# Performance work log

Hardware: AMD Instinct MI355X
Metric: run time of the kernel (lower is better)

## Reference

```python
import jax, jax.numpy as jnp
import numpy as np

B, L, H, NH, NB = 16, 200, 128, 2, 2
ITEMS, SPAN = 50000, 256
NEG = -2.0**32 + 1.0  # mask value used by the torch module


def _ln(x, g, b, eps=1e-8):
    m = jnp.mean(x, axis=-1, keepdims=True)
    v = jnp.mean((x - m) ** 2, axis=-1, keepdims=True)
    return (x - m) / jnp.sqrt(v + eps) * g + b


def setup_inputs() -> dict:
    key = jax.random.key(0)
    ks = jax.random.split(key, 20)
    p = lambda k, s: (jax.random.normal(k, s, jnp.float32) * 0.02)
    item_emb = p(ks[0], (ITEMS + 1, H)).at[0].set(0.0)  # padding_idx=0
    return {
        "user_ids": jax.random.randint(ks[1], (B,), 0, 10000),
        "log_seqs": jax.random.randint(ks[2], (B, L), 0, ITEMS),
        "time_matrices": jax.random.randint(ks[3], (B, L, L), 0, SPAN),
        "pos_seqs": jax.random.randint(ks[4], (B, L), 0, ITEMS),
        "neg_seqs": jax.random.randint(ks[5], (B, L), 0, ITEMS),
        "item_emb": item_emb,
        "pos_K_emb": p(ks[6], (L, H)),
        "pos_V_emb": p(ks[7], (L, H)),
        "time_K_emb": p(ks[8], (SPAN + 1, H)),
        "time_V_emb": p(ks[9], (SPAN + 1, H)),
        "Wq": p(ks[10], (NB, H, H)), "bq": jnp.zeros((NB, H)),
        "Wk": p(ks[11], (NB, H, H)), "bk": jnp.zeros((NB, H)),
        "Wv": p(ks[12], (NB, H, H)), "bv": jnp.zeros((NB, H)),
        "ln1_g": jnp.ones((NB, H)), "ln1_b": jnp.zeros((NB, H)),
        "W1": p(ks[13], (NB, H, H)), "b1": jnp.zeros((NB, H)),
        "W2": p(ks[14], (NB, H, H)), "b2": jnp.zeros((NB, H)),
        "ln2_g": jnp.ones((NB, H)), "ln2_b": jnp.zeros((NB, H)),
        "lnf_g": jnp.ones((H,)), "lnf_b": jnp.zeros((H,)),
    }


def reference(user_ids, log_seqs, time_matrices, pos_seqs, neg_seqs,
              item_emb, pos_K_emb, pos_V_emb, time_K_emb, time_V_emb,
              Wq, bq, Wk, bk, Wv, bv, ln1_g, ln1_b,
              W1, b1, W2, b2, ln2_g, ln2_b, lnf_g, lnf_b):
    d = H // NH
    pad = (log_seqs == 0)                    # (B,L) timeline mask
    keep = (~pad)[..., None].astype(jnp.float32)

    seqs = item_emb[log_seqs] * jnp.sqrt(jnp.float32(H))
    seqs = seqs * keep
    posK = pos_K_emb.reshape(L, NH, d)       # same for every batch element
    posV = pos_V_emb.reshape(L, NH, d)
    tmK = time_K_emb[time_matrices].reshape(B, L, L, NH, d)  # (B,L,L,h,d)
    tmV = time_V_emb[time_matrices].reshape(B, L, L, NH, d)
    causal = ~jnp.tril(jnp.ones((L, L), dtype=bool))          # True = masked
    mask = pad[:, None, :, None] | causal[None, None, :, :]   # (B,1,L,L) row-mask | causal

    for i in range(NB):
        Q = (seqs @ Wq[i].T + bq[i]).reshape(B, L, NH, d)
        K = (seqs @ Wk[i].T + bk[i]).reshape(B, L, NH, d)
        V = (seqs @ Wv[i].T + bv[i]).reshape(B, L, NH, d)
        aw = jnp.einsum('bqhd,bkhd->bhqk', Q, K)
        aw = aw + jnp.einsum('bqhd,khd->bhqk', Q, posK)
        aw = aw + jnp.einsum('bqkhd,bqhd->bhqk', tmK, Q)
        aw = aw / jnp.sqrt(jnp.float32(d))
        aw = jnp.where(mask, NEG, aw)
        A = jax.nn.softmax(aw, axis=-1)                        # (B,h,L,L)
        out = jnp.einsum('bhqk,bkhd->bqhd', A, V)
        out = out + jnp.einsum('bhqk,khd->bqhd', A, posV)
        out = out + jnp.einsum('bhqk,bqkhd->bqhd', A, tmV)
        out = out.reshape(B, L, H)
        seqs = _ln(seqs + out, ln1_g[i], ln1_b[i])
        ffn = jax.nn.relu(seqs @ W1[i].T + b1[i]) @ W2[i].T + b2[i]
        seqs = _ln(seqs + ffn, ln2_g[i], ln2_b[i])
        seqs = seqs * keep

    log_feats = _ln(seqs, lnf_g, lnf_b)
    pos_logits = jnp.sum(log_feats * item_emb[pos_seqs], axis=-1)  # (B,L)
    neg_logits = jnp.sum(log_feats * item_emb[neg_seqs], axis=-1)
    return jnp.stack([pos_logits, neg_logits])  # (2,B,L)
```

## Files before the change

kernel.cpp:

```cpp
#include <hip/hip_runtime.h>
#include <hip/hip_bf16.h>
#include <math.h>

#define BB 16
#define LL 200
#define HH 128
#define DD 64
#define NQT 25
#define NEGF -4294967295.0f
#define SQRTH 11.313708498984761f

__global__ __launch_bounds__(512) void k_qkv(float* __restrict__ seqs,
    const int* __restrict__ log_seqs, const float* __restrict__ item_emb, int do_embed,
    const float* __restrict__ Wq, const float* __restrict__ bq,
    const float* __restrict__ Wk, const float* __restrict__ bk,
    const float* __restrict__ Wv, const float* __restrict__ bv,
    const float* __restrict__ posK, const float* __restrict__ posV,
    float* __restrict__ Q, float* __restrict__ Kp, float* __restrict__ Vp) {
    __shared__ float s_lds[16][HH];
    int r0g = blockIdx.x * 16;
    int t = threadIdx.x;
    if (do_embed) {
        int r = t >> 5, d4 = t & 31;
        int id = log_seqs[r0g + r];
        float4 v = make_float4(0.f, 0.f, 0.f, 0.f);
        if (id != 0) {
            v = ((const float4*)(item_emb + id * HH))[d4];
            v.x *= SQRTH; v.y *= SQRTH; v.z *= SQRTH; v.w *= SQRTH;
        }
        *(float4*)&s_lds[r][d4 * 4] = v;
        ((float4*)(seqs + r0g * HH))[t] = v;
    } else {
        ((float4*)s_lds)[t] = ((const float4*)(seqs + r0g * HH))[t];
    }
    __syncthreads();
    int c = t & 127, rg = t >> 7;
    float aq[4] = {0.f, 0.f, 0.f, 0.f};
    float ak[4] = {0.f, 0.f, 0.f, 0.f};
    float av[4] = {0.f, 0.f, 0.f, 0.f};
    const float4* wq4 = (const float4*)(Wq + c * HH);
    const float4* wk4 = (const float4*)(Wk + c * HH);
    const float4* wv4 = (const float4*)(Wv + c * HH);
#pragma unroll 4
    for (int k4 = 0; k4 < HH / 4; ++k4) {
        float4 wq = wq4[k4], wk = wk4[k4], wv = wv4[k4];
#pragma unroll
        for (int r = 0; r < 4; ++r) {
            float4 s = *(const float4*)&s_lds[rg * 4 + r][k4 * 4];
            aq[r] += s.x * wq.x + s.y * wq.y + s.z * wq.z + s.w * wq.w;
            ak[r] += s.x * wk.x + s.y * wk.y + s.z * wk.z + s.w * wk.w;
            av[r] += s.x * wv.x + s.y * wv.y + s.z * wv.z + s.w * wv.w;
        }
    }
#pragma unroll
    for (int r = 0; r < 4; ++r) {
        int row = r0g + rg * 4 + r;
        int l = row % LL;
        Q[row * HH + c]  = aq[r] + bq[c];
        Kp[row * HH + c] = ak[r] + bk[c] + posK[l * HH + c];
        Vp[row * HH + c] = av[r] + bv[c] + posV[l * HH + c];
    }
}

__global__ __launch_bounds__(256) void k_proj(const float* __restrict__ Q,
    const float* __restrict__ timeK, float* __restrict__ projK) {
    int bh = blockIdx.x / 25, qt = blockIdx.x % 25;
    int b = bh >> 1, h = bh & 1;
    int qlo = qt * 8;
    __shared__ float Qs[8][68];
    __shared__ float TK[2][32][68];
    int t = threadIdx.x;
    if (t < 128) {
        int r = t >> 4, d4 = t & 15;
        *(float4*)&Qs[r][d4 * 4] =
            ((const float4*)(Q + (b * LL + qlo + r) * HH + h * DD))[d4];
    }
    for (int x = t; x < 512; x += 256) {
        int i = x >> 4, d4 = x & 15;
        *(float4*)&TK[0][i][d4 * 4] =
            ((const float4*)(timeK + i * HH + h * DD))[d4];
    }
    int tq = t >> 5, ttl = t & 31;
    for (int ch = 0; ch < 9; ++ch) {
        __syncthreads();
        if (ch + 1 < 9) {
            int nb = (ch + 1) * 32;
            for (int x = t; x < 512; x += 256) {
                int i = x >> 4, d4 = x & 15;
                int tt = nb + i;
                if (tt < 257)
                    *(float4*)&TK[(ch + 1) & 1][i][d4 * 4] =
                        ((const float4*)(timeK + tt * HH + h * DD))[d4];
            }
        }
        int tt = ch * 32 + ttl;
        if (tt < 257) {
            float acc = 0.f;
#pragma unroll
            for (int d4 = 0; d4 < 16; ++d4) {
                float4 qv = *(const float4*)&Qs[tq][d4 * 4];
                float4 kv = *(const float4*)&TK[ch & 1][ttl][d4 * 4];
                acc += qv.x * kv.x + qv.y * kv.y + qv.z * kv.z + qv.w * kv.w;
            }
            projK[(bh * LL + qlo + tq) * 257 + tt] = acc;
        }
    }
}

__global__ __launch_bounds__(256) void k_attn(
    const float* __restrict__ Q, const float* __restrict__ Kp, const float* __restrict__ Vp,
    const float* __restrict__ projK, const float* __restrict__ timeV,
    const int* __restrict__ tm, const int* __restrict__ log_seqs,
    float* __restrict__ attnout) {
    int bh = blockIdx.x / NQT, qt = blockIdx.x % NQT;
    int b = bh >> 1, h = bh & 1;
    int qlo = qt * 8;
    __shared__ float K_s[2][32][68];
    __shared__ float smemW[457 * 12];
    __shared__ int s_allmask;
#define WT(i, j) smemW[(i) * 12 + (j)]
    int t = threadIdx.x;
    int tq = t >> 5, lane = t & 31, g = tq;
    int q = qlo + tq;
    int qhi = qlo + 7;

    if (t == 0) s_allmask = 0;
    for (int x = 200 * 12 + t; x < 457 * 12; x += 256) smemW[x] = 0.f;
    float4 qreg[16];
    {
        const float4* qp = (const float4*)(Q + (b * LL + q) * HH + h * DD);
#pragma unroll
        for (int d4 = 0; d4 < 16; ++d4) qreg[d4] = qp[d4];
    }
    const int* tmrow = tm + (b * LL + q) * LL;
    const float* projrow = projK + (bh * LL + q) * 257;
    const int* lsrow = log_seqs + b * LL;

    for (int x = t; x < 512; x += 256) {
        int i = x >> 4, d4 = x & 15;
        *(float4*)&K_s[0][i][d4 * 4] =
            ((const float4*)(Kp + (b * LL + i) * HH + h * DD))[d4];
    }

    float s[7];
#pragma unroll
    for (int j = 0; j < 7; ++j) s[j] = NEGF;
    int nkc = (qhi >> 5) + 1;
#pragma unroll
    for (int kc = 0; kc < 7; ++kc) {
        if (kc < nkc) {
            __syncthreads();
            if (kc + 1 < nkc) {
                int kb = (kc + 1) * 32;
                for (int x = t; x < 512; x += 256) {
                    int i = x >> 4, d4 = x & 15;
                    int k = kb + i;
                    if (k < LL)
                        *(float4*)&K_s[(kc + 1) & 1][i][d4 * 4] =
                            ((const float4*)(Kp + (b * LL + k) * HH + h * DD))[d4];
                }
            }
            int k = kc * 32 + lane;
            if (k <= q && lsrow[k] != 0) {
                float acc = 0.f;
#pragma unroll
                for (int d4 = 0; d4 < 16; ++d4) {
                    float4 kv = *(const float4*)&K_s[kc & 1][lane][d4 * 4];
                    acc += qreg[d4].x * kv.x + qreg[d4].y * kv.y +
                           qreg[d4].z * kv.z + qreg[d4].w * kv.w;
                }
                s[kc] = (acc + projrow[tmrow[k]]) * 0.125f;
            }
        }
    }

    float mx = s[0];
#pragma unroll
    for (int j = 1; j < 7; ++j) mx = fmaxf(mx, s[j]);
    mx = fmaxf(mx, __shfl_xor(mx, 1, 64));
    mx = fmaxf(mx, __shfl_xor(mx, 2, 64));
    mx = fmaxf(mx, __shfl_xor(mx, 4, 64));
    mx = fmaxf(mx, __shfl_xor(mx, 8, 64));
    mx = fmaxf(mx, __shfl_xor(mx, 16, 64));
    bool allmask = (mx == NEGF);
    float sum = 0.f;
#pragma unroll
    for (int j = 0; j < 7; ++j) {
        int k = lane + 32 * j;
        float e = (k < LL) ? __expf(s[j] - mx) : 0.f;
        s[j] = e;
        sum += e;
    }
    sum += __shfl_xor(sum, 1, 64);
    sum += __shfl_xor(sum, 2, 64);
    sum += __shfl_xor(sum, 4, 64);
    sum += __shfl_xor(sum, 8, 64);
    sum += __shfl_xor(sum, 16, 64);
    float inv = 1.0f / sum;
    int klim = allmask ? LL : (q + 1);
    if (allmask && lane == 0) s_allmask = 1;
#pragma unroll
    for (int j = 0; j < 7; ++j) {
        int k = lane + 32 * j;
        if (k < LL) {
            float p = s[j] * inv;
            WT(k, tq) = p;
            if (k < klim && p != 0.f)
                atomicAdd(&WT(200 + tmrow[k], tq), p);
        }
    }
    __syncthreads();

    int kmax = s_allmask ? LL : (qhi + 1);
    float a00=0.f,a01=0.f,a10=0.f,a11=0.f,a20=0.f,a21=0.f,a30=0.f,a31=0.f;
    float a40=0.f,a41=0.f,a50=0.f,a51=0.f,a60=0.f,a61=0.f,a70=0.f,a71=0.f;
#define PV_STEP(WROW, SRCPTR)                                            \
    {                                                                    \
        const float* wr = &WROW;                                         \
        float4 w0 = *(const float4*)wr;                                  \
        float4 w1 = *(const float4*)(wr + 4);                            \
        float2 vv = *(const float2*)(SRCPTR);                            \
        a00 += w0.x * vv.x; a01 += w0.x * vv.y;                          \
        a10 += w0.y * vv.x; a11 += w0.y * vv.y;                          \
        a20 += w0.z * vv.x; a21 += w0.z * vv.y;                          \
        a30 += w0.w * vv.x; a31 += w0.w * vv.y;                          \
        a40 += w1.x * vv.x; a41 += w1.x * vv.y;                          \
        a50 += w1.y * vv.x; a51 += w1.y * vv.y;                          \
        a60 += w1.z * vv.x; a61 += w1.z * vv.y;                          \
        a70 += w1.w * vv.x; a71 += w1.w * vv.y;                          \
    }
    for (int i = g; i < kmax; i += 8)
        PV_STEP(WT(i, 0), Vp + (b * LL + i) * HH + h * DD + lane * 2);
    for (int i = g; i < 257; i += 8)
        PV_STEP(WT(200 + i, 0), timeV + i * HH + h * DD + lane * 2);
#undef PV_STEP
    __syncthreads();
    float* part = smemW;
    part[g * 512 + 0 * 64 + lane * 2] = a00; part[g * 512 + 0 * 64 + lane * 2 + 1] = a01;
    part[g * 512 + 1 * 64 + lane * 2] = a10; part[g * 512 + 1 * 64 + lane * 2 + 1] = a11;
    part[g * 512 + 2 * 64 + lane * 2] = a20; part[g * 512 + 2 * 64 + lane * 2 + 1] = a21;
    part[g * 512 + 3 * 64 + lane * 2] = a30; part[g * 512 + 3 * 64 + lane * 2 + 1] = a31;
    part[g * 512 + 4 * 64 + lane * 2] = a40; part[g * 512 + 4 * 64 + lane * 2 + 1] = a41;
    part[g * 512 + 5 * 64 + lane * 2] = a50; part[g * 512 + 5 * 64 + lane * 2 + 1] = a51;
    part[g * 512 + 6 * 64 + lane * 2] = a60; part[g * 512 + 6 * 64 + lane * 2 + 1] = a61;
    part[g * 512 + 7 * 64 + lane * 2] = a70; part[g * 512 + 7 * 64 + lane * 2 + 1] = a71;
    __syncthreads();
    {
        float ox = 0.f, oy = 0.f;
#pragma unroll
        for (int gg = 0; gg < 8; ++gg) {
            ox += part[gg * 512 + tq * 64 + lane * 2];
            oy += part[gg * 512 + tq * 64 + lane * 2 + 1];
        }
        *(float2*)(attnout + (b * LL + q) * HH + h * DD + lane * 2) =
            make_float2(ox, oy);
    }
#undef WT
}

__global__ __launch_bounds__(512) void k_ffn_full(
    float* __restrict__ seqs, const float* __restrict__ AO,
    const float* __restrict__ g1, const float* __restrict__ be1,
    const float* __restrict__ W1, const float* __restrict__ b1,
    const float* __restrict__ W2, const float* __restrict__ b2,
    const float* __restrict__ g2, const float* __restrict__ be2,
    const int* __restrict__ log_seqs, int do_final,
    const float* __restrict__ lnf_g, const float* __restrict__ lnf_b,
    const float* __restrict__ item_emb,
    const int* __restrict__ pos_seqs, const int* __restrict__ neg_seqs,
    float* __restrict__ out) {
    __shared__ float s_lds[16][HH];
    __shared__ float h_lds[16][HH];
    int r0g = blockIdx.x * 16;
    int t = threadIdx.x;
    {
        float4 a = ((const float4*)(seqs + r0g * HH))[t];
        float4 o = ((const float4*)(AO + r0g * HH))[t];
        a.x += o.x; a.y += o.y; a.z += o.z; a.w += o.w;
        ((float4*)s_lds)[t] = a;
    }
    __syncthreads();
    int w = t >> 6, lane = t & 63;
    int lrow = w * 2 + (lane >> 5), cl = lane & 31;
    {
        float sm = 0.f;
#pragma unroll
        for (int j = 0; j < 4; ++j) sm += s_lds[lrow][cl + 32 * j];
        sm += __shfl_xor(sm, 1, 64);  sm += __shfl_xor(sm, 2, 64);
        sm += __shfl_xor(sm, 4, 64);  sm += __shfl_xor(sm, 8, 64);
        sm += __shfl_xor(sm, 16, 64);
        float mean = sm * (1.0f / HH);
        float vr = 0.f;
#pragma unroll
        for (int j = 0; j < 4; ++j) {
            float d = s_lds[lrow][cl + 32 * j] - mean;
            vr += d * d;
        }
        vr += __shfl_xor(vr, 1, 64);  vr += __shfl_xor(vr, 2, 64);
        vr += __shfl_xor(vr, 4, 64);  vr += __shfl_xor(vr, 8, 64);
        vr += __shfl_xor(vr, 16, 64);
        float rstd = rsqrtf(vr * (1.0f / HH) + 1e-8f);
#pragma unroll
        for (int j = 0; j < 4; ++j) {
            int c = cl + 32 * j;
            s_lds[lrow][c] = (s_lds[lrow][c] - mean) * rstd * g1[c] + be1[c];
        }
    }
    __syncthreads();
    int c = t & 127, rg = t >> 7;
    float acc[4] = {0.f, 0.f, 0.f, 0.f};
    const float4* w14 = (const float4*)(W1 + c * HH);
#pragma unroll 4
    for (int k4 = 0; k4 < HH / 4; ++k4) {
        float4 ww = w14[k4];
#pragma unroll
        for (int r = 0; r < 4; ++r) {
            float4 s = *(const float4*)&s_lds[rg * 4 + r][k4 * 4];
            acc[r] += s.x * ww.x + s.y * ww.y + s.z * ww.z + s.w * ww.w;
        }
    }
#pragma unroll
    for (int r = 0; r < 4; ++r) h_lds[rg * 4 + r][c] = fmaxf(acc[r] + b1[c], 0.f);
    __syncthreads();
#pragma unroll
    for (int r = 0; r < 4; ++r) acc[r] = 0.f;
    const float4* w24 = (const float4*)(W2 + c * HH);
#pragma unroll 4
    for (int k4 = 0; k4 < HH / 4; ++k4) {
        float4 ww = w24[k4];
#pragma unroll
        for (int r = 0; r < 4; ++r) {
            float4 s = *(const float4*)&h_lds[rg * 4 + r][k4 * 4];
            acc[r] += s.x * ww.x + s.y * ww.y + s.z * ww.z + s.w * ww.w;
        }
    }
    __syncthreads();
#pragma unroll
    for (int r = 0; r < 4; ++r)
        h_lds[rg * 4 + r][c] = s_lds[rg * 4 + r][c] + acc[r] + b2[c];
    __syncthreads();
    {
        float sm = 0.f;
#pragma unroll
        for (int j = 0; j < 4; ++j) sm += h_lds[lrow][cl + 32 * j];
        sm += __shfl_xor(sm, 1, 64);  sm += __shfl_xor(sm, 2, 64);
        sm += __shfl_xor(sm, 4, 64);  sm += __shfl_xor(sm, 8, 64);
        sm += __shfl_xor(sm, 16, 64);
        float mean = sm * (1.0f / HH);
        float vr = 0.f;
#pragma unroll
        for (int j = 0; j < 4; ++j) {
            float d = h_lds[lrow][cl + 32 * j] - mean;
            vr += d * d;
        }
        vr += __shfl_xor(vr, 1, 64);  vr += __shfl_xor(vr, 2, 64);
        vr += __shfl_xor(vr, 4, 64);  vr += __shfl_xor(vr, 8, 64);
        vr += __shfl_xor(vr, 16, 64);
        float rstd = rsqrtf(vr * (1.0f / HH) + 1e-8f);
        int row = r0g + lrow;
        float keep = (log_seqs[row] != 0) ? 1.0f : 0.0f;
        float y2[4];
#pragma unroll
        for (int j = 0; j < 4; ++j) {
            int cc = cl + 32 * j;
            y2[j] = ((h_lds[lrow][cc] - mean) * rstd * g2[cc] + be2[cc]) * keep;
        }
        if (!do_final) {
#pragma unroll
            for (int j = 0; j < 4; ++j)
                seqs[row * HH + cl + 32 * j] = y2[j];
        } else {
            float sm2 = y2[0] + y2[1] + y2[2] + y2[3];
            sm2 += __shfl_xor(sm2, 1, 64);  sm2 += __shfl_xor(sm2, 2, 64);
            sm2 += __shfl_xor(sm2, 4, 64);  sm2 += __shfl_xor(sm2, 8, 64);
            sm2 += __shfl_xor(sm2, 16, 64);
            float mean2 = sm2 * (1.0f / HH);
            float vr2 = 0.f;
#pragma unroll
            for (int j = 0; j < 4; ++j) {
                float d = y2[j] - mean2;
                vr2 += d * d;
            }
            vr2 += __shfl_xor(vr2, 1, 64);  vr2 += __shfl_xor(vr2, 2, 64);
            vr2 += __shfl_xor(vr2, 4, 64);  vr2 += __shfl_xor(vr2, 8, 64);
            vr2 += __shfl_xor(vr2, 16, 64);
            float rstd2 = rsqrtf(vr2 * (1.0f / HH) + 1e-8f);
            int pid = pos_seqs[row];
            int nid = neg_seqs[row];
            float pp = 0.f, nn = 0.f;
#pragma unroll
            for (int j = 0; j < 4; ++j) {
                int cc = cl + 32 * j;
                float lf = (y2[j] - mean2) * rstd2 * lnf_g[cc] + lnf_b[cc];
                pp += lf * item_emb[pid * HH + cc];
                nn += lf * item_emb[nid * HH + cc];
            }
            pp += __shfl_xor(pp, 1, 64);  pp += __shfl_xor(pp, 2, 64);
            pp += __shfl_xor(pp, 4, 64);  pp += __shfl_xor(pp, 8, 64);
            pp += __shfl_xor(pp, 16, 64);
            nn += __shfl_xor(nn, 1, 64);  nn += __shfl_xor(nn, 2, 64);
            nn += __shfl_xor(nn, 4, 64);  nn += __shfl_xor(nn, 8, 64);
            nn += __shfl_xor(nn, 16, 64);
            if (cl == 0) {
                out[row] = pp;
                out[BB * LL + row] = nn;
            }
        }
    }
}

extern "C" void kernel_launch(void* const* d_in, const int* in_sizes, int n_in,
                              void* d_out, int out_size, void* d_ws, size_t ws_size,
                              hipStream_t stream) {
    const int* log_seqs = (const int*)d_in[1];
    const int* tm       = (const int*)d_in[2];
    const int* pos_seqs = (const int*)d_in[3];
    const int* neg_seqs = (const int*)d_in[4];
    const float* item_emb = (const float*)d_in[5];
    const float* posK   = (const float*)d_in[6];
    const float* posV   = (const float*)d_in[7];
    const float* timeK  = (const float*)d_in[8];
    const float* timeV  = (const float*)d_in[9];
    const float* Wq = (const float*)d_in[10];
    const float* bq = (const float*)d_in[11];
    const float* Wk = (const float*)d_in[12];
    const float* bk = (const float*)d_in[13];
    const float* Wv = (const float*)d_in[14];
    const float* bv = (const float*)d_in[15];
    const float* ln1_g = (const float*)d_in[16];
    const float* ln1_b = (const float*)d_in[17];
    const float* W1 = (const float*)d_in[18];
    const float* b1 = (const float*)d_in[19];
    const float* W2 = (const float*)d_in[20];
    const float* b2 = (const float*)d_in[21];
    const float* ln2_g = (const float*)d_in[22];
    const float* ln2_b = (const float*)d_in[23];
    const float* lnf_g = (const float*)d_in[24];
    const float* lnf_b = (const float*)d_in[25];

    float* ws    = (float*)d_ws;
    float* seqs  = ws;
    float* Qb    = seqs + 409600;
    float* Kpb   = Qb + 409600;
    float* Vpb   = Kpb + 409600;
    float* AO    = Vpb + 409600;
    float* projK = AO + 409600;

    for (int i = 0; i < 2; ++i) {
        k_qkv<<<BB * LL / 16, 512, 0, stream>>>(seqs, log_seqs, item_emb,
            (i == 0) ? 1 : 0,
            Wq + i * HH * HH, bq + i * HH,
            Wk + i * HH * HH, bk + i * HH,
            Wv + i * HH * HH, bv + i * HH,
            posK, posV, Qb, Kpb, Vpb);
        k_proj<<<32 * NQT, 256, 0, stream>>>(Qb, timeK, projK);
        k_attn<<<32 * NQT, 256, 0, stream>>>(Qb, Kpb, Vpb, projK, timeV,
                                             tm, log_seqs, AO);
        k_ffn_full<<<BB * LL / 16, 512, 0, stream>>>(seqs, AO,
            ln1_g + i * HH, ln1_b + i * HH,
            W1 + i * HH * HH, b1 + i * HH,
            W2 + i * HH * HH, b2 + i * HH,
            ln2_g + i * HH, ln2_b + i * HH, log_seqs,
            (i == 1) ? 1 : 0, lnf_g, lnf_b, item_emb,
            pos_seqs, neg_seqs, (float*)d_out);
    }
}
```

Before: 186.1 us.

## Fuse all layer stages into one cooperative persistent kernel with grid syncs

Replaces the eight separate kernel launches (qkv, proj, attn, ffn for each of two layers) with a single cooperative persistent kernel that loops over tiles and uses grid-wide barriers between phases. The goal is to remove per-launch overhead and the idle gaps between dependent kernels. In exchange, all phases now run with 256 threads and 8-row tiles instead of 512 threads and 16-row tiles. The attention K-tile loading also loses its double buffering and adds an extra barrier per chunk. Grid-sync cost and the reduced occupancy, set by the shared smem footprint, could offset the gains.

```diff
diff --git a/kernel.cpp b/kernel.cpp
--- a/kernel.cpp
+++ b/kernel.cpp
@@ -1,6 +1,8 @@
 #include <hip/hip_runtime.h>
-#include <hip/hip_bf16.h>
+#include <hip/hip_cooperative_groups.h>
 #include <math.h>
+
+namespace cg = cooperative_groups;
 
 #define BB 16
 #define LL 200
@@ -10,30 +12,42 @@
 #define NEGF -4294967295.0f
 #define SQRTH 11.313708498984761f
 
-__global__ __launch_bounds__(512) void k_qkv(float* __restrict__ seqs,
-    const int* __restrict__ log_seqs, const float* __restrict__ item_emb, int do_embed,
-    const float* __restrict__ Wq, const float* __restrict__ bq,
-    const float* __restrict__ Wk, const float* __restrict__ bk,
-    const float* __restrict__ Wv, const float* __restrict__ bv,
-    const float* __restrict__ posK, const float* __restrict__ posV,
-    float* __restrict__ Q, float* __restrict__ Kp, float* __restrict__ Vp) {
-    __shared__ float s_lds[16][HH];
-    int r0g = blockIdx.x * 16;
+struct Params {
+    const int* log_seqs; const int* tm; const int* pos_seqs; const int* neg_seqs;
+    const float* item_emb; const float* posK; const float* posV;
+    const float* timeK; const float* timeV;
+    const float* Wq; const float* bq; const float* Wk; const float* bk;
+    const float* Wv; const float* bv;
+    const float* ln1_g; const float* ln1_b;
+    const float* W1; const float* b1; const float* W2; const float* b2;
+    const float* ln2_g; const float* ln2_b;
+    const float* lnf_g; const float* lnf_b;
+    float* seqs; float* Q; float* Kp; float* Vp; float* AO; float* projK;
+    float* out;
+};
+
+__device__ void ph_qkv(const Params& P, float* smem, int tile, int layer) {
+    float (*s_lds)[HH] = (float (*)[HH])smem;
+    int r0g = tile * 8;
     int t = threadIdx.x;
-    if (do_embed) {
+    __syncthreads();
+    if (layer == 0) {
         int r = t >> 5, d4 = t & 31;
-        int id = log_seqs[r0g + r];
+        int id = P.log_seqs[r0g + r];
         float4 v = make_float4(0.f, 0.f, 0.f, 0.f);
         if (id != 0) {
-            v = ((const float4*)(item_emb + id * HH))[d4];
+            v = ((const float4*)(P.item_emb + id * HH))[d4];
             v.x *= SQRTH; v.y *= SQRTH; v.z *= SQRTH; v.w *= SQRTH;
         }
         *(float4*)&s_lds[r][d4 * 4] = v;
-        ((float4*)(seqs + r0g * HH))[t] = v;
+        ((float4*)(P.seqs + r0g * HH))[t] = v;
     } else {
-        ((float4*)s_lds)[t] = ((const float4*)(seqs + r0g * HH))[t];
-    }
-    __syncthreads();
+        ((float4*)s_lds)[t] = ((const float4*)(P.seqs + r0g * HH))[t];
+    }
+    __syncthreads();
+    const float* Wq = P.Wq + layer * HH * HH; const float* bq = P.bq + layer * HH;
+    const float* Wk = P.Wk + layer * HH * HH; const float* bk = P.bk + layer * HH;
+    const float* Wv = P.Wv + layer * HH * HH; const float* bv = P.bv + layer * HH;
     int c = t & 127, rg = t >> 7;
     float aq[4] = {0.f, 0.f, 0.f, 0.f};
     float ak[4] = {0.f, 0.f, 0.f, 0.f};
@@ -56,29 +70,29 @@
     for (int r = 0; r < 4; ++r) {
         int row = r0g + rg * 4 + r;
         int l = row % LL;
-        Q[row * HH + c]  = aq[r] + bq[c];
-        Kp[row * HH + c] = ak[r] + bk[c] + posK[l * HH + c];
-        Vp[row * HH + c] = av[r] + bv[c] + posV[l * HH + c];
-    }
-}
-
-__global__ __launch_bounds__(256) void k_proj(const float* __restrict__ Q,
-    const float* __restrict__ timeK, float* __restrict__ projK) {
-    int bh = blockIdx.x / 25, qt = blockIdx.x % 25;
+        P.Q[row * HH + c]  = aq[r] + bq[c];
+        P.Kp[row * HH + c] = ak[r] + bk[c] + P.posK[l * HH + c];
+        P.Vp[row * HH + c] = av[r] + bv[c] + P.posV[l * HH + c];
+    }
+}
+
+__device__ void ph_proj(const Params& P, float* smem, int tile) {
+    float (*Qs)[68] = (float (*)[68])smem;
+    float (*TK)[32][68] = (float (*)[32][68])(smem + 544);
+    int bh = tile / NQT, qt = tile % NQT;
     int b = bh >> 1, h = bh & 1;
     int qlo = qt * 8;
-    __shared__ float Qs[8][68];
-    __shared__ float TK[2][32][68];
     int t = threadIdx.x;
+    __syncthreads();
     if (t < 128) {
         int r = t >> 4, d4 = t & 15;
         *(float4*)&Qs[r][d4 * 4] =
-            ((const float4*)(Q + (b * LL + qlo + r) * HH + h * DD))[d4];
+            ((const float4*)(P.Q + (b * LL + qlo + r) * HH + h * DD))[d4];
     }
     for (int x = t; x < 512; x += 256) {
         int i = x >> 4, d4 = x & 15;
         *(float4*)&TK[0][i][d4 * 4] =
-            ((const float4*)(timeK + i * HH + h * DD))[d4];
+            ((const float4*)(P.timeK + i * HH + h * DD))[d4];
     }
     int tq = t >> 5, ttl = t & 31;
     for (int ch = 0; ch < 9; ++ch) {
@@ -90,7 +104,7 @@
                 int tt = nb + i;
                 if (tt < 257)
                     *(float4*)&TK[(ch + 1) & 1][i][d4 * 4] =
-                        ((const float4*)(timeK + tt * HH + h * DD))[d4];
+                        ((const float4*)(P.timeK + tt * HH + h * DD))[d4];
             }
         }
         int tt = ch * 32 + ttl;
@@ -102,45 +116,34 @@
                 float4 kv = *(const float4*)&TK[ch & 1][ttl][d4 * 4];
                 acc += qv.x * kv.x + qv.y * kv.y + qv.z * kv.z + qv.w * kv.w;
             }
-            projK[(bh * LL + qlo + tq) * 257 + tt] = acc;
-        }
-    }
-}
-
-__global__ __launch_bounds__(256) void k_attn(
-    const float* __restrict__ Q, const float* __restrict__ Kp, const float* __restrict__ Vp,
-    const float* __restrict__ projK, const float* __restrict__ timeV,
-    const int* __restrict__ tm, const int* __restrict__ log_seqs,
-    float* __restrict__ attnout) {
-    int bh = blockIdx.x / NQT, qt = blockIdx.x % NQT;
+            P.projK[(bh * LL + qlo + tq) * 257 + tt] = acc;
+        }
+    }
+}
+
+__device__ void ph_attn(const Params& P, float* smem, int* s_allmask_p, int tile) {
+    float (*K_s)[68] = (float (*)[68])smem;
+    float* smemW = smem + 2176;
+#define WT(i, j) smemW[(i) * 12 + (j)]
+    int bh = tile / NQT, qt = tile % NQT;
     int b = bh >> 1, h = bh & 1;
     int qlo = qt * 8;
-    __shared__ float K_s[2][32][68];
-    __shared__ float smemW[457 * 12];
-    __shared__ int s_allmask;
-#define WT(i, j) smemW[(i) * 12 + (j)]
     int t = threadIdx.x;
     int tq = t >> 5, lane = t & 31, g = tq;
     int q = qlo + tq;
     int qhi = qlo + 7;
-
-    if (t == 0) s_allmask = 0;
+    __syncthreads();
+    if (t == 0) *s_allmask_p = 0;
     for (int x = 200 * 12 + t; x < 457 * 12; x += 256) smemW[x] = 0.f;
     float4 qreg[16];
     {
-        const float4* qp = (const float4*)(Q + (b * LL + q) * HH + h * DD);
+        const float4* qp = (const float4*)(P.Q + (b * LL + q) * HH + h * DD);
 #pragma unroll
         for (int d4 = 0; d4 < 16; ++d4) qreg[d4] = qp[d4];
     }
-    const int* tmrow = tm + (b * LL + q) * LL;
-    const float* projrow = projK + (bh * LL + q) * 257;
-    const int* lsrow = log_seqs + b * LL;
-
-    for (int x = t; x < 512; x += 256) {
-        int i = x >> 4, d4 = x & 15;
-        *(float4*)&K_s[0][i][d4 * 4] =
-            ((const float4*)(Kp + (b * LL + i) * HH + h * DD))[d4];
-    }
+    const int* tmrow = P.tm + (b * LL + q) * LL;
+    const float* projrow = P.projK + (bh * LL + q) * 257;
+    const int* lsrow = P.log_seqs + b * LL;
 
     float s[7];
 #pragma unroll
@@ -149,28 +152,27 @@
 #pragma unroll
     for (int kc = 0; kc < 7; ++kc) {
         if (kc < nkc) {
+            int kbase = kc * 32;
+            for (int x = t; x < 512; x += 256) {
+                int i = x >> 4, d4 = x & 15;
+                int k = kbase + i;
+                if (k < LL)
+                    *(float4*)&K_s[i][d4 * 4] =
+                        ((const float4*)(P.Kp + (b * LL + k) * HH + h * DD))[d4];
+            }
             __syncthreads();
-            if (kc + 1 < nkc) {
-                int kb = (kc + 1) * 32;
-                for (int x = t; x < 512; x += 256) {
-                    int i = x >> 4, d4 = x & 15;
-                    int k = kb + i;
-                    if (k < LL)
-                        *(float4*)&K_s[(kc + 1) & 1][i][d4 * 4] =
-                            ((const float4*)(Kp + (b * LL + k) * HH + h * DD))[d4];
-                }
-            }
-            int k = kc * 32 + lane;
+            int k = kbase + lane;
             if (k <= q && lsrow[k] != 0) {
                 float acc = 0.f;
 #pragma unroll
                 for (int d4 = 0; d4 < 16; ++d4) {
-                    float4 kv = *(const float4*)&K_s[kc & 1][lane][d4 * 4];
+                    float4 kv = *(const float4*)&K_s[lane][d4 * 4];
                     acc += qreg[d4].x * kv.x + qreg[d4].y * kv.y +
                            qreg[d4].z * kv.z + qreg[d4].w * kv.w;
                 }
                 s[kc] = (acc + projrow[tmrow[k]]) * 0.125f;
             }
+            __syncthreads();
         }
     }
 
@@ -198,7 +200,7 @@
     sum += __shfl_xor(sum, 16, 64);
     float inv = 1.0f / sum;
     int klim = allmask ? LL : (q + 1);
-    if (allmask && lane == 0) s_allmask = 1;
+    if (allmask && lane == 0) *s_allmask_p = 1;
 #pragma unroll
     for (int j = 0; j < 7; ++j) {
         int k = lane + 32 * j;
@@ -211,7 +213,7 @@
     }
     __syncthreads();
 
-    int kmax = s_allmask ? LL : (qhi + 1);
+    int kmax = (*s_allmask_p) ? LL : (qhi + 1);
     float a00=0.f,a01=0.f,a10=0.f,a11=0.f,a20=0.f,a21=0.f,a30=0.f,a31=0.f;
     float a40=0.f,a41=0.f,a50=0.f,a51=0.f,a60=0.f,a61=0.f,a70=0.f,a71=0.f;
 #define PV_STEP(WROW, SRCPTR)                                            \
@@ -230,9 +232,9 @@
         a70 += w1.w * vv.x; a71 += w1.w * vv.y;                          \
     }
     for (int i = g; i < kmax; i += 8)
-        PV_STEP(WT(i, 0), Vp + (b * LL + i) * HH + h * DD + lane * 2);
+        PV_STEP(WT(i, 0), P.Vp + (b * LL + i) * HH + h * DD + lane * 2);
     for (int i = g; i < 257; i += 8)
-        PV_STEP(WT(200 + i, 0), timeV + i * HH + h * DD + lane * 2);
+        PV_STEP(WT(200 + i, 0), P.timeV + i * HH + h * DD + lane * 2);
 #undef PV_STEP
     __syncthreads();
     float* part = smemW;
@@ -252,30 +254,26 @@
             ox += part[gg * 512 + tq * 64 + lane * 2];
             oy += part[gg * 512 + tq * 64 + lane * 2 + 1];
         }
-        *(float2*)(attnout + (b * LL + q) * HH + h * DD + lane * 2) =
+        *(float2*)(P.AO + (b * LL + q) * HH + h * DD + lane * 2) =
             make_float2(ox, oy);
     }
 #undef WT
 }
 
-__global__ __launch_bounds__(512) void k_ffn_full(
-    float* __restrict__ seqs, const float* __restrict__ AO,
-    const float* __restrict__ g1, const float* __restrict__ be1,
-    const float* __restrict__ W1, const float* __restrict__ b1,
-    const float* __restrict__ W2, const float* __restrict__ b2,
-    const float* __restrict__ g2, const float* __restrict__ be2,
-    const int* __restrict__ log_seqs, int do_final,
-    const float* __restrict__ lnf_g, const float* __restrict__ lnf_b,
-    const float* __restrict__ item_emb,
-    const int* __restrict__ pos_seqs, const int* __restrict__ neg_seqs,
-    float* __restrict__ out) {
-    __shared__ float s_lds[16][HH];
-    __shared__ float h_lds[16][HH];
-    int r0g = blockIdx.x * 16;
+__device__ void ph_ffn(const Params& P, float* smem, int tile, int layer) {
+    float (*s_lds)[HH] = (float (*)[HH])smem;
+    float (*h_lds)[HH] = (float (*)[HH])(smem + 1024);
+    int r0g = tile * 8;
     int t = threadIdx.x;
+    int do_final = (layer == 1);
+    const float* g1  = P.ln1_g + layer * HH; const float* be1 = P.ln1_b + layer * HH;
+    const float* W1  = P.W1 + layer * HH * HH; const float* b1 = P.b1 + layer * HH;
+    const float* W2  = P.W2 + layer * HH * HH; const float* b2 = P.b2 + layer * HH;
+    const float* g2  = P.ln2_g + layer * HH; const float* be2 = P.ln2_b + layer * HH;
+    __syncthreads();
     {
-        float4 a = ((const float4*)(seqs + r0g * HH))[t];
-        float4 o = ((const float4*)(AO + r0g * HH))[t];
+        float4 a = ((const float4*)(P.seqs + r0g * HH))[t];
+        float4 o = ((const float4*)(P.AO + r0g * HH))[t];
         a.x += o.x; a.y += o.y; a.z += o.z; a.w += o.w;
         ((float4*)s_lds)[t] = a;
     }
@@ -358,7 +356,7 @@
         vr += __shfl_xor(vr, 16, 64);
         float rstd = rsqrtf(vr * (1.0f / HH) + 1e-8f);
         int row = r0g + lrow;
-        float keep = (log_seqs[row] != 0) ? 1.0f : 0.0f;
+        float keep = (P.log_seqs[row] != 0) ? 1.0f : 0.0f;
         float y2[4];
 #pragma unroll
         for (int j = 0; j < 4; ++j) {
@@ -368,7 +366,7 @@
         if (!do_final) {
 #pragma unroll
             for (int j = 0; j < 4; ++j)
-                seqs[row * HH + cl + 32 * j] = y2[j];
+                P.seqs[row * HH + cl + 32 * j] = y2[j];
         } else {
             float sm2 = y2[0] + y2[1] + y2[2] + y2[3];
             sm2 += __shfl_xor(sm2, 1, 64);  sm2 += __shfl_xor(sm2, 2, 64);
@@ -385,15 +383,15 @@
             vr2 += __shfl_xor(vr2, 4, 64);  vr2 += __shfl_xor(vr2, 8, 64);
             vr2 += __shfl_xor(vr2, 16, 64);
             float rstd2 = rsqrtf(vr2 * (1.0f / HH) + 1e-8f);
-            int pid = pos_seqs[row];
-            int nid = neg_seqs[row];
+            int pid = P.pos_seqs[row];
+            int nid = P.neg_seqs[row];
             float pp = 0.f, nn = 0.f;
 #pragma unroll
             for (int j = 0; j < 4; ++j) {
                 int cc = cl + 32 * j;
-                float lf = (y2[j] - mean2) * rstd2 * lnf_g[cc] + lnf_b[cc];
-                pp += lf * item_emb[pid * HH + cc];
-                nn += lf * item_emb[nid * HH + cc];
+                float lf = (y2[j] - mean2) * rstd2 * P.lnf_g[cc] + P.lnf_b[cc];
+                pp += lf * P.item_emb[pid * HH + cc];
+                nn += lf * P.item_emb[nid * HH + cc];
             }
             pp += __shfl_xor(pp, 1, 64);  pp += __shfl_xor(pp, 2, 64);
             pp += __shfl_xor(pp, 4, 64);  pp += __shfl_xor(pp, 8, 64);
@@ -402,66 +400,72 @@
             nn += __shfl_xor(nn, 4, 64);  nn += __shfl_xor(nn, 8, 64);
             nn += __shfl_xor(nn, 16, 64);
             if (cl == 0) {
-                out[row] = pp;
-                out[BB * LL + row] = nn;
-            }
-        }
+                P.out[row] = pp;
+                P.out[BB * LL + row] = nn;
+            }
+        }
+    }
+}
+
+__global__ __launch_bounds__(256, 4) void k_mega(Params P) {
+    cg::grid_group grid = cg::this_grid();
+    __shared__ float smem[7660];
+    __shared__ int s_allmask;
+    for (int layer = 0; layer < 2; ++layer) {
+        for (int tile = blockIdx.x; tile < 400; tile += gridDim.x)
+            ph_qkv(P, smem, tile, layer);
+        grid.sync();
+        for (int tile = blockIdx.x; tile < 800; tile += gridDim.x)
+            ph_proj(P, smem, tile);
+        grid.sync();
+        for (int tile = blockIdx.x; tile < 800; tile += gridDim.x)
+            ph_attn(P, smem, &s_allmask, tile);
+        grid.sync();
+        for (int tile = blockIdx.x; tile < 400; tile += gridDim.x)
+            ph_ffn(P, smem, tile, layer);
+        if (layer == 0) grid.sync();
     }
 }
 
 extern "C" void kernel_launch(void* const* d_in, const int* in_sizes, int n_in,
                               void* d_out, int out_size, void* d_ws, size_t ws_size,
                               hipStream_t stream) {
-    const int* log_seqs = (const int*)d_in[1];
-    const int* tm       = (const int*)d_in[2];
-    const int* pos_seqs = (const int*)d_in[3];
-    const int* neg_seqs = (const int*)d_in[4];
-    const float* item_emb = (const float*)d_in[5];
-    const float* posK   = (const float*)d_in[6];
-    const float* posV   = (const float*)d_in[7];
-    const float* timeK  = (const float*)d_in[8];
-    const float* timeV  = (const float*)d_in[9];
-    const float* Wq = (const float*)d_in[10];
-    const float* bq = (const float*)d_in[11];
-    const float* Wk = (const float*)d_in[12];
-    const float* bk = (const float*)d_in[13];
-    const float* Wv = (const float*)d_in[14];
-    const float* bv = (const float*)d_in[15];
-    const float* ln1_g = (const float*)d_in[16];
-    const float* ln1_b = (const float*)d_in[17];
-    const float* W1 = (const float*)d_in[18];
-    const float* b1 = (const float*)d_in[19];
-    const float* W2 = (const float*)d_in[20];
-    const float* b2 = (const float*)d_in[21];
-    const float* ln2_g = (const float*)d_in[22];
-    const float* ln2_b = (const float*)d_in[23];
-    const float* lnf_g = (const float*)d_in[24];
-    const float* lnf_b = (const float*)d_in[25];
-
-    float* ws    = (float*)d_ws;
-    float* seqs  = ws;
-    float* Qb    = seqs + 409600;
-    float* Kpb   = Qb + 409600;
-    float* Vpb   = Kpb + 409600;
-    float* AO    = Vpb + 409600;
-    float* projK = AO + 409600;
-
-    for (int i = 0; i < 2; ++i) {
-        k_qkv<<<BB * LL / 16, 512, 0, stream>>>(seqs, log_seqs, item_emb,
-            (i == 0) ? 1 : 0,
-            Wq + i * HH * HH, bq + i * HH,
-            Wk + i * HH * HH, bk + i * HH,
-            Wv + i * HH * HH, bv + i * HH,
-            posK, posV, Qb, Kpb, Vpb);
-        k_proj<<<32 * NQT, 256, 0, stream>>>(Qb, timeK, projK);
-        k_attn<<<32 * NQT, 256, 0, stream>>>(Qb, Kpb, Vpb, projK, timeV,
-                                             tm, log_seqs, AO);
-        k_ffn_full<<<BB * LL / 16, 512, 0, stream>>>(seqs, AO,
-            ln1_g + i * HH, ln1_b + i * HH,
-            W1 + i * HH * HH, b1 + i * HH,
-            W2 + i * HH * HH, b2 + i * HH,
-            ln2_g + i * HH, ln2_b + i * HH, log_seqs,
-            (i == 1) ? 1 : 0, lnf_g, lnf_b, item_emb,
-            pos_seqs, neg_seqs, (float*)d_out);
-    }
-}
+    Params P;
+    P.log_seqs = (const int*)d_in[1];
+    P.tm       = (const int*)d_in[2];
+    P.pos_seqs = (const int*)d_in[3];
+    P.neg_seqs = (const int*)d_in[4];
+    P.item_emb = (const float*)d_in[5];
+    P.posK  = (const float*)d_in[6];
+    P.posV  = (const float*)d_in[7];
+    P.timeK = (const float*)d_in[8];
+    P.timeV = (const float*)d_in[9];
+    P.Wq = (const float*)d_in[10]; P.bq = (const float*)d_in[11];
+    P.Wk = (const float*)d_in[12]; P.bk = (const float*)d_in[13];
+    P.Wv = (const float*)d_in[14]; P.bv = (const float*)d_in[15];
+    P.ln1_g = (const float*)d_in[16]; P.ln1_b = (const float*)d_in[17];
+    P.W1 = (const float*)d_in[18]; P.b1 = (const float*)d_in[19];
+    P.W2 = (const float*)d_in[20]; P.b2 = (const float*)d_in[21];
+    P.ln2_g = (const float*)d_in[22]; P.ln2_b = (const float*)d_in[23];
+    P.lnf_g = (const float*)d_in[24]; P.lnf_b = (const float*)d_in[25];
+
+    float* ws = (float*)d_ws;
+    P.seqs  = ws;
+    P.Q     = ws + 409600;
+    P.Kp    = ws + 2 * 409600;
+    P.Vp    = ws + 3 * 409600;
+    P.AO    = ws + 4 * 409600;
+    P.projK = ws + 5 * 409600;
+    P.out   = (float*)d_out;
+
+    int maxBlk = 0;
+    if (hipOccupancyMaxActiveBlocksPerMultiprocessor(&maxBlk, (const void*)k_mega,
+                                                     256, 0) != hipSuccess || maxBlk < 1)
+        maxBlk = 1;
+    unsigned grid = (unsigned)maxBlk * 256u;
+    if (grid > 800u) grid = 800u;
+
+    void* args[] = { (void*)&P };
+    hipLaunchCooperativeKernel((const void*)k_mega, dim3(grid), dim3(256),
+                               args, 0, stream);
+}
```

Measured after the change: 660.4 us. 3.55x slower.

## Drop double buffering in proj/attn and retile FFN to four rows per block

Applied to the files above, without the earlier changes.

The time-embedding and key tile loads in k_proj and k_attn go from double-buffered prefetch to single-buffered load-then-sync loops, which halves their shared memory but removes load/compute overlap and adds a barrier per chunk. The FFN kernel now handles 4 rows per 512-thread block instead of 16, so it launches 800 blocks instead of 200. Each thread computes one output column for one row, and layernorm reductions span the full 64-lane wavefront. More blocks spread the work across more CUs, but W1/W2 reuse per block drops fourfold.

```diff
diff --git a/kernel.cpp b/kernel.cpp
--- a/kernel.cpp
+++ b/kernel.cpp
@@ -68,38 +68,32 @@
     int b = bh >> 1, h = bh & 1;
     int qlo = qt * 8;
     __shared__ float Qs[8][68];
-    __shared__ float TK[2][32][68];
+    __shared__ float TK[32][68];
     int t = threadIdx.x;
     if (t < 128) {
         int r = t >> 4, d4 = t & 15;
         *(float4*)&Qs[r][d4 * 4] =
             ((const float4*)(Q + (b * LL + qlo + r) * HH + h * DD))[d4];
     }
-    for (int x = t; x < 512; x += 256) {
-        int i = x >> 4, d4 = x & 15;
-        *(float4*)&TK[0][i][d4 * 4] =
-            ((const float4*)(timeK + i * HH + h * DD))[d4];
-    }
     int tq = t >> 5, ttl = t & 31;
     for (int ch = 0; ch < 9; ++ch) {
+        int base = ch * 32;
         __syncthreads();
-        if (ch + 1 < 9) {
-            int nb = (ch + 1) * 32;
-            for (int x = t; x < 512; x += 256) {
-                int i = x >> 4, d4 = x & 15;
-                int tt = nb + i;
-                if (tt < 257)
-                    *(float4*)&TK[(ch + 1) & 1][i][d4 * 4] =
-                        ((const float4*)(timeK + tt * HH + h * DD))[d4];
-            }
-        }
-        int tt = ch * 32 + ttl;
+        for (int x = t; x < 512; x += 256) {
+            int i = x >> 4, d4 = x & 15;
+            int tt = base + i;
+            if (tt < 257)
+                *(float4*)&TK[i][d4 * 4] =
+                    ((const float4*)(timeK + tt * HH + h * DD))[d4];
+        }
+        __syncthreads();
+        int tt = base + ttl;
         if (tt < 257) {
             float acc = 0.f;
 #pragma unroll
             for (int d4 = 0; d4 < 16; ++d4) {
                 float4 qv = *(const float4*)&Qs[tq][d4 * 4];
-                float4 kv = *(const float4*)&TK[ch & 1][ttl][d4 * 4];
+                float4 kv = *(const float4*)&TK[ttl][d4 * 4];
                 acc += qv.x * kv.x + qv.y * kv.y + qv.z * kv.z + qv.w * kv.w;
             }
             projK[(bh * LL + qlo + tq) * 257 + tt] = acc;
@@ -115,7 +109,7 @@
     int bh = blockIdx.x / NQT, qt = blockIdx.x % NQT;
     int b = bh >> 1, h = bh & 1;
     int qlo = qt * 8;
-    __shared__ float K_s[2][32][68];
+    __shared__ float K_s[32][68];
     __shared__ float smemW[457 * 12];
     __shared__ int s_allmask;
 #define WT(i, j) smemW[(i) * 12 + (j)]
@@ -136,12 +130,6 @@
     const float* projrow = projK + (bh * LL + q) * 257;
     const int* lsrow = log_seqs + b * LL;
 
-    for (int x = t; x < 512; x += 256) {
-        int i = x >> 4, d4 = x & 15;
-        *(float4*)&K_s[0][i][d4 * 4] =
-            ((const float4*)(Kp + (b * LL + i) * HH + h * DD))[d4];
-    }
-
     float s[7];
 #pragma unroll
     for (int j = 0; j < 7; ++j) s[j] = NEGF;
@@ -149,28 +137,27 @@
 #pragma unroll
     for (int kc = 0; kc < 7; ++kc) {
         if (kc < nkc) {
+            int kbase = kc * 32;
+            for (int x = t; x < 512; x += 256) {
+                int i = x >> 4, d4 = x & 15;
+                int k = kbase + i;
+                if (k < LL)
+                    *(float4*)&K_s[i][d4 * 4] =
+                        ((const float4*)(Kp + (b * LL + k) * HH + h * DD))[d4];
+            }
             __syncthreads();
-            if (kc + 1 < nkc) {
-                int kb = (kc + 1) * 32;
-                for (int x = t; x < 512; x += 256) {
-                    int i = x >> 4, d4 = x & 15;
-                    int k = kb + i;
-                    if (k < LL)
-                        *(float4*)&K_s[(kc + 1) & 1][i][d4 * 4] =
-                            ((const float4*)(Kp + (b * LL + k) * HH + h * DD))[d4];
-                }
-            }
-            int k = kc * 32 + lane;
+            int k = kbase + lane;
             if (k <= q && lsrow[k] != 0) {
                 float acc = 0.f;
 #pragma unroll
                 for (int d4 = 0; d4 < 16; ++d4) {
-                    float4 kv = *(const float4*)&K_s[kc & 1][lane][d4 * 4];
+                    float4 kv = *(const float4*)&K_s[lane][d4 * 4];
                     acc += qreg[d4].x * kv.x + qreg[d4].y * kv.y +
                            qreg[d4].z * kv.z + qreg[d4].w * kv.w;
                 }
                 s[kc] = (acc + projrow[tmrow[k]]) * 0.125f;
             }
+            __syncthreads();
         }
     }
 
@@ -258,7 +245,7 @@
 #undef WT
 }
 
-__global__ __launch_bounds__(512) void k_ffn_full(
+__global__ __launch_bounds__(512) void k_ffn(
     float* __restrict__ seqs, const float* __restrict__ AO,
     const float* __restrict__ g1, const float* __restrict__ be1,
     const float* __restrict__ W1, const float* __restrict__ b1,
@@ -269,141 +256,116 @@
     const float* __restrict__ item_emb,
     const int* __restrict__ pos_seqs, const int* __restrict__ neg_seqs,
     float* __restrict__ out) {
-    __shared__ float s_lds[16][HH];
-    __shared__ float h_lds[16][HH];
-    int r0g = blockIdx.x * 16;
+    __shared__ float s_lds[4][HH];
+    __shared__ float h_lds[4][HH];
+    int r0g = blockIdx.x * 4;
     int t = threadIdx.x;
-    {
+    int wv = t >> 6, lane = t & 63;
+    int lrow = wv >> 1, par = wv & 1;
+
+    if (t < 128) {
         float4 a = ((const float4*)(seqs + r0g * HH))[t];
         float4 o = ((const float4*)(AO + r0g * HH))[t];
         a.x += o.x; a.y += o.y; a.z += o.z; a.w += o.w;
         ((float4*)s_lds)[t] = a;
     }
     __syncthreads();
-    int w = t >> 6, lane = t & 63;
-    int lrow = w * 2 + (lane >> 5), cl = lane & 31;
-    {
-        float sm = 0.f;
-#pragma unroll
-        for (int j = 0; j < 4; ++j) sm += s_lds[lrow][cl + 32 * j];
+    {
+        float x0 = s_lds[lrow][lane], x1 = s_lds[lrow][lane + 64];
+        float sm = x0 + x1;
         sm += __shfl_xor(sm, 1, 64);  sm += __shfl_xor(sm, 2, 64);
         sm += __shfl_xor(sm, 4, 64);  sm += __shfl_xor(sm, 8, 64);
-        sm += __shfl_xor(sm, 16, 64);
+        sm += __shfl_xor(sm, 16, 64); sm += __shfl_xor(sm, 32, 64);
         float mean = sm * (1.0f / HH);
-        float vr = 0.f;
-#pragma unroll
-        for (int j = 0; j < 4; ++j) {
-            float d = s_lds[lrow][cl + 32 * j] - mean;
-            vr += d * d;
-        }
+        float d0 = x0 - mean, d1 = x1 - mean;
+        float vr = d0 * d0 + d1 * d1;
         vr += __shfl_xor(vr, 1, 64);  vr += __shfl_xor(vr, 2, 64);
         vr += __shfl_xor(vr, 4, 64);  vr += __shfl_xor(vr, 8, 64);
-        vr += __shfl_xor(vr, 16, 64);
+        vr += __shfl_xor(vr, 16, 64); vr += __shfl_xor(vr, 32, 64);
         float rstd = rsqrtf(vr * (1.0f / HH) + 1e-8f);
-#pragma unroll
-        for (int j = 0; j < 4; ++j) {
-            int c = cl + 32 * j;
-            s_lds[lrow][c] = (s_lds[lrow][c] - mean) * rstd * g1[c] + be1[c];
-        }
-    }
-    __syncthreads();
-    int c = t & 127, rg = t >> 7;
-    float acc[4] = {0.f, 0.f, 0.f, 0.f};
-    const float4* w14 = (const float4*)(W1 + c * HH);
-#pragma unroll 4
-    for (int k4 = 0; k4 < HH / 4; ++k4) {
-        float4 ww = w14[k4];
-#pragma unroll
-        for (int r = 0; r < 4; ++r) {
-            float4 s = *(const float4*)&s_lds[rg * 4 + r][k4 * 4];
-            acc[r] += s.x * ww.x + s.y * ww.y + s.z * ww.z + s.w * ww.w;
-        }
-    }
-#pragma unroll
-    for (int r = 0; r < 4; ++r) h_lds[rg * 4 + r][c] = fmaxf(acc[r] + b1[c], 0.f);
-    __syncthreads();
-#pragma unroll
-    for (int r = 0; r < 4; ++r) acc[r] = 0.f;
-    const float4* w24 = (const float4*)(W2 + c * HH);
-#pragma unroll 4
-    for (int k4 = 0; k4 < HH / 4; ++k4) {
-        float4 ww = w24[k4];
-#pragma unroll
-        for (int r = 0; r < 4; ++r) {
-            float4 s = *(const float4*)&h_lds[rg * 4 + r][k4 * 4];
-            acc[r] += s.x * ww.x + s.y * ww.y + s.z * ww.z + s.w * ww.w;
-        }
-    }
-    __syncthreads();
-#pragma unroll
-    for (int r = 0; r < 4; ++r)
-        h_lds[rg * 4 + r][c] = s_lds[rg * 4 + r][c] + acc[r] + b2[c];
-    __syncthreads();
-    {
-        float sm = 0.f;
-#pragma unroll
-        for (int j = 0; j < 4; ++j) sm += h_lds[lrow][cl + 32 * j];
+        int cw = lane + par * 64;
+        float dn = par ? d1 : d0;
+        __syncthreads();
+        s_lds[lrow][cw] = dn * rstd * g1[cw] + be1[cw];
+    }
+    __syncthreads();
+    int row = t >> 7, col = t & 127;
+    {
+        float acc = 0.f;
+        const float4* w4 = (const float4*)(W1 + col * HH);
+        const float4* s4 = (const float4*)&s_lds[row][0];
+#pragma unroll 8
+        for (int k4 = 0; k4 < 32; ++k4) {
+            float4 w = w4[k4];
+            float4 s = s4[k4];
+            acc += s.x * w.x + s.y * w.y + s.z * w.z + s.w * w.w;
+        }
+        h_lds[row][col] = fmaxf(acc + b1[col], 0.f);
+    }
+    __syncthreads();
+    float x2;
+    {
+        float acc = 0.f;
+        const float4* w4 = (const float4*)(W2 + col * HH);
+        const float4* h4 = (const float4*)&h_lds[row][0];
+#pragma unroll 8
+        for (int k4 = 0; k4 < 32; ++k4) {
+            float4 w = w4[k4];
+            float4 s = h4[k4];
+            acc += s.x * w.x + s.y * w.y + s.z * w.z + s.w * w.w;
+        }
+        x2 = s_lds[row][col] + acc + b2[col];
+    }
+    __syncthreads();
+    h_lds[row][col] = x2;
+    __syncthreads();
+    {
+        float x0 = h_lds[lrow][lane], x1 = h_lds[lrow][lane + 64];
+        float sm = x0 + x1;
         sm += __shfl_xor(sm, 1, 64);  sm += __shfl_xor(sm, 2, 64);
         sm += __shfl_xor(sm, 4, 64);  sm += __shfl_xor(sm, 8, 64);
-        sm += __shfl_xor(sm, 16, 64);
+        sm += __shfl_xor(sm, 16, 64); sm += __shfl_xor(sm, 32, 64);
         float mean = sm * (1.0f / HH);
-        float vr = 0.f;
-#pragma unroll
-        for (int j = 0; j < 4; ++j) {
-            float d = h_lds[lrow][cl + 32 * j] - mean;
-            vr += d * d;
-        }
+        float d0 = x0 - mean, d1 = x1 - mean;
+        float vr = d0 * d0 + d1 * d1;
         vr += __shfl_xor(vr, 1, 64);  vr += __shfl_xor(vr, 2, 64);
         vr += __shfl_xor(vr, 4, 64);  vr += __shfl_xor(vr, 8, 64);
-        vr += __shfl_xor(vr, 16, 64);
+        vr += __shfl_xor(vr, 16, 64); vr += __shfl_xor(vr, 32, 64);
         float rstd = rsqrtf(vr * (1.0f / HH) + 1e-8f);
-        int row = r0g + lrow;
-        float keep = (log_seqs[row] != 0) ? 1.0f : 0.0f;
-        float y2[4];
-#pragma unroll
-        for (int j = 0; j < 4; ++j) {
-            int cc = cl + 32 * j;
-            y2[j] = ((h_lds[lrow][cc] - mean) * rstd * g2[cc] + be2[cc]) * keep;
-        }
+        int grow = r0g + lrow;
+        float keep = (log_seqs[grow] != 0) ? 1.0f : 0.0f;
+        float y0 = (d0 * rstd * g2[lane] + be2[lane]) * keep;
+        float y1 = (d1 * rstd * g2[lane + 64] + be2[lane + 64]) * keep;
         if (!do_final) {
-#pragma unroll
-            for (int j = 0; j < 4; ++j)
-                seqs[row * HH + cl + 32 * j] = y2[j];
+            if (par == 0) seqs[grow * HH + lane] = y0;
+            else          seqs[grow * HH + lane + 64] = y1;
         } else {
-            float sm2 = y2[0] + y2[1] + y2[2] + y2[3];
+            float sm2 = y0 + y1;
             sm2 += __shfl_xor(sm2, 1, 64);  sm2 += __shfl_xor(sm2, 2, 64);
             sm2 += __shfl_xor(sm2, 4, 64);  sm2 += __shfl_xor(sm2, 8, 64);
-            sm2 += __shfl_xor(sm2, 16, 64);
+            sm2 += __shfl_xor(sm2, 16, 64); sm2 += __shfl_xor(sm2, 32, 64);
             float mean2 = sm2 * (1.0f / HH);
-            float vr2 = 0.f;
-#pragma unroll
-            for (int j = 0; j < 4; ++j) {
-                float d = y2[j] - mean2;
-                vr2 += d * d;
-            }
+            float e0 = y0 - mean2, e1 = y1 - mean2;
+            float vr2 = e0 * e0 + e1 * e1;
             vr2 += __shfl_xor(vr2, 1, 64);  vr2 += __shfl_xor(vr2, 2, 64);
             vr2 += __shfl_xor(vr2, 4, 64);  vr2 += __shfl_xor(vr2, 8, 64);
-            vr2 += __shfl_xor(vr2, 16, 64);
+            vr2 += __shfl_xor(vr2, 16, 64); vr2 += __shfl_xor(vr2, 32, 64);
             float rstd2 = rsqrtf(vr2 * (1.0f / HH) + 1e-8f);
-            int pid = pos_seqs[row];
-            int nid = neg_seqs[row];
-            float pp = 0.f, nn = 0.f;
-#pragma unroll
-            for (int j = 0; j < 4; ++j) {
-                int cc = cl + 32 * j;
-                float lf = (y2[j] - mean2) * rstd2 * lnf_g[cc] + lnf_b[cc];
-                pp += lf * item_emb[pid * HH + cc];
-                nn += lf * item_emb[nid * HH + cc];
-            }
+            int pid = pos_seqs[grow];
+            int nid = neg_seqs[grow];
+            float lf0 = e0 * rstd2 * lnf_g[lane] + lnf_b[lane];
+            float lf1 = e1 * rstd2 * lnf_g[lane + 64] + lnf_b[lane + 64];
+            float pp = lf0 * item_emb[pid * HH + lane] + lf1 * item_emb[pid * HH + lane + 64];
+            float nn = lf0 * item_emb[nid * HH + lane] + lf1 * item_emb[nid * HH + lane + 64];
             pp += __shfl_xor(pp, 1, 64);  pp += __shfl_xor(pp, 2, 64);
             pp += __shfl_xor(pp, 4, 64);  pp += __shfl_xor(pp, 8, 64);
-            pp += __shfl_xor(pp, 16, 64);
+            pp += __shfl_xor(pp, 16, 64); pp += __shfl_xor(pp, 32, 64);
             nn += __shfl_xor(nn, 1, 64);  nn += __shfl_xor(nn, 2, 64);
             nn += __shfl_xor(nn, 4, 64);  nn += __shfl_xor(nn, 8, 64);
-            nn += __shfl_xor(nn, 16, 64);
-            if (cl == 0) {
-                out[row] = pp;
-                out[BB * LL + row] = nn;
+            nn += __shfl_xor(nn, 16, 64); nn += __shfl_xor(nn, 32, 64);
+            if (par == 0 && lane == 0) {
+                out[grow] = pp;
+                out[BB * LL + grow] = nn;
             }
         }
     }
@@ -456,7 +418,7 @@
         k_proj<<<32 * NQT, 256, 0, stream>>>(Qb, timeK, projK);
         k_attn<<<32 * NQT, 256, 0, stream>>>(Qb, Kpb, Vpb, projK, timeV,
                                              tm, log_seqs, AO);
-        k_ffn_full<<<BB * LL / 16, 512, 0, stream>>>(seqs, AO,
+        k_ffn<<<BB * LL / 4, 512, 0, stream>>>(seqs, AO,
             ln1_g + i * HH, ln1_b + i * HH,
             W1 + i * HH * HH, b1 + i * HH,
             W2 + i * HH * HH, b2 + i * HH,
```

After: 266.9 us. +43.4%, slower.
